# Optimization experiments

Measured on AMD Instinct MI355X. Metric: run time of the kernel, lower is better.

The kernel has to match this reference:

```python
import jax, jax.numpy as jnp
import numpy as np

B, T, D, HEADS = 2, 2048, 1024, 16


def setup_inputs() -> dict:
    key = jax.random.key(0)
    k1, k2, k3 = jax.random.split(key, 3)
    X = jax.random.normal(k1, (B, T, D), dtype=jnp.float32)
    W_KQV = jax.random.normal(k2, (D, 3 * D), dtype=jnp.float32) * 0.02
    W_out = jax.random.normal(k3, (D, D), dtype=jnp.float32) * 0.02
    # causal additive mask: -1e9 above the diagonal, 0 elsewhere
    mask = jnp.triu(jnp.full((T, T), -1e9, dtype=jnp.float32), k=1)
    return {"X": X, "W_KQV": W_KQV, "W_out": W_out, "mask": mask, "heads": HEADS}


def reference(X, W_KQV, W_out, mask, heads):
    b, t, d = X.shape
    hd = d // heads
    res = jnp.einsum('btd,de->bte', X, W_KQV)  # [B,T,3d]
    # needle module stacks split columns in K, Q, V order
    K, Q, V = jnp.split(res, 3, axis=-1)

    def to_heads(A):  # [B,T,d] -> [B,H,T,hd]
        return A.reshape(b, t, heads, hd).transpose(0, 2, 1, 3)

    K, Q, V = to_heads(K), to_heads(Q), to_heads(V)
    # NOTE: original computes K @ Q^T (not Q @ K^T) -- reproduced faithfully
    scores = jnp.einsum('bhkd,bhqd->bhkq', K, Q) / (hd ** 0.5) + mask  # [B,H,T,T]
    attn = jax.nn.softmax(scores, axis=-1)
    ctx = jnp.einsum('bhtq,bhqd->bhtd', attn, V)  # [B,H,T,hd]
    ctx = ctx.transpose(0, 2, 1, 3).reshape(b, t, d)
    out = jnp.einsum('btd,de->bte', ctx, W_out)  # [B,T,d]
    return out, attn
```

## Files before the change

### kernel.cpp

```cpp
#include <hip/hip_runtime.h>
#include <cstddef>

constexpr int B_ = 2, T_ = 2048, D_ = 1024, H_ = 16;

typedef __attribute__((ext_vector_type(8))) short short8;
typedef __attribute__((ext_vector_type(4))) float floatx4;

__device__ inline unsigned short f2bf(float f) {
    union { float f; unsigned int u; } v; v.f = f;
    unsigned int r = v.u + 0x7fffu + ((v.u >> 16) & 1u);
    return (unsigned short)(r >> 16);
}

#define GLD_LDS16(gptr, ldsptr)                                                        \
    __builtin_amdgcn_global_load_lds(                                                  \
        (const __attribute__((address_space(1))) void*)(gptr),                         \
        (__attribute__((address_space(3))) void*)(ldsptr), 16, 0, 0)

__global__ __launch_bounds__(256) void cast_bf16(const float* __restrict__ in,
                                                 unsigned short* __restrict__ out) {
    int idx = (blockIdx.x * 256 + threadIdx.x) * 8;
    float4 a = *(const float4*)(in + idx);
    float4 b = *(const float4*)(in + idx + 4);
    unsigned short tmp[8] = {f2bf(a.x), f2bf(a.y), f2bf(a.z), f2bf(a.w),
                             f2bf(b.x), f2bf(b.y), f2bf(b.z), f2bf(b.w)};
    *(uint4*)(out + idx) = *(const uint4*)tmp;
}

__global__ __launch_bounds__(256) void transpose_cast(const float* __restrict__ W,
                                                      unsigned short* __restrict__ Wt,
                                                      int K, int N) {
    const int k0 = blockIdx.y * 64, n0 = blockIdx.x * 64;
    __shared__ float t[64][65];
    const int tid = threadIdx.x;
    const int row = tid >> 4, c4 = (tid & 15) * 4;
#pragma unroll
    for (int r = 0; r < 4; r++) {
        float4 v = *(const float4*)&W[(size_t)(k0 + row + r * 16) * N + n0 + c4];
        t[row + r * 16][c4 + 0] = v.x; t[row + r * 16][c4 + 1] = v.y;
        t[row + r * 16][c4 + 2] = v.z; t[row + r * 16][c4 + 3] = v.w;
    }
    __syncthreads();
    const int n = tid >> 2, ks = (tid & 3) * 16;
    unsigned short o[16];
#pragma unroll
    for (int i = 0; i < 16; i++) o[i] = f2bf(t[ks + i][n]);
    unsigned short* dst = Wt + (size_t)(n0 + n) * K + k0 + ks;
    *(uint4*)dst = ((const uint4*)o)[0];
    *(uint4*)(dst + 8) = ((const uint4*)o)[1];
}

template <typename CT>
__global__ __launch_bounds__(256, 2) void gemm_bt(const unsigned short* __restrict__ A,
                                                  const unsigned short* __restrict__ Bt,
                                                  CT* __restrict__ C, int M, int N, int K) {
    __shared__ unsigned short As[128 * 64];
    __shared__ unsigned short Bs[128 * 64];
    const int tid = threadIdx.x;
    const int lane = tid & 63, wave = tid >> 6;
    const int quad = lane >> 4, l16 = lane & 15;
    const int wr = wave >> 1, wc = wave & 1;
    const size_t bm = (size_t)blockIdx.y * 128, bn = (size_t)blockIdx.x * 128;
    const unsigned short* Ap = A + bm * K;
    const unsigned short* Bp = Bt + bn * K;
    const int srow = tid >> 3, sc = tid & 7;
    floatx4 acc[4][4] = {};
    for (int k0 = 0; k0 < K; k0 += 64) {
#pragma unroll
        for (int it = 0; it < 4; it++) {
            int rr = srow + it * 32;
            int soff = k0 + ((sc ^ (rr & 7)) << 3);
            GLD_LDS16(Ap + (size_t)rr * K + soff, &As[(tid + it * 256) * 8]);
            GLD_LDS16(Bp + (size_t)rr * K + soff, &Bs[(tid + it * 256) * 8]);
        }
        __syncthreads();
#pragma unroll
        for (int ks = 0; ks < 2; ks++) {
            short8 af[4], bf[4];
#pragma unroll
            for (int i = 0; i < 4; i++) {
                int row = wr * 64 + i * 16 + l16, cf = ks * 4 + quad;
                af[i] = *(const short8*)&As[row * 64 + ((cf ^ (row & 7)) << 3)];
            }
#pragma unroll
            for (int j = 0; j < 4; j++) {
                int row = wc * 64 + j * 16 + l16, cf = ks * 4 + quad;
                bf[j] = *(const short8*)&Bs[row * 64 + ((cf ^ (row & 7)) << 3)];
            }
#pragma unroll
            for (int i = 0; i < 4; i++)
#pragma unroll
                for (int j = 0; j < 4; j++)
                    acc[i][j] = __builtin_amdgcn_mfma_f32_16x16x32_bf16(af[i], bf[j], acc[i][j], 0, 0, 0);
        }
        __syncthreads();
    }
#pragma unroll
    for (int i = 0; i < 4; i++) {
        size_t row0 = bm + wr * 64 + i * 16 + quad * 4;
#pragma unroll
        for (int j = 0; j < 4; j++) {
            size_t col = bn + wc * 64 + j * 16 + l16;
#pragma unroll
            for (int r = 0; r < 4; r++) {
                if constexpr (sizeof(CT) == 2)
                    C[(row0 + r) * N + col] = (CT)f2bf(acc[i][j][r]);
                else
                    C[(row0 + r) * N + col] = acc[i][j][r];
            }
        }
    }
}

__global__ __launch_bounds__(256) void transpose_v(const unsigned short* __restrict__ resb,
                                                   unsigned short* __restrict__ Vt) {
    const int bh = blockIdx.y, b = bh >> 4, h = bh & 15;
    const int q0 = blockIdx.x * 64;
    __shared__ unsigned short t[64][66];
    const int tid = threadIdx.x;
    const unsigned short* Vg = resb + (size_t)b * T_ * (3 * D_) + 2 * D_ + h * 64;
    const int q = tid >> 3, c8 = (tid & 7) * 8;
#pragma unroll
    for (int r = 0; r < 2; r++) {
        int qq = q + r * 32;
        short8 v = *(const short8*)(Vg + (size_t)(q0 + qq) * (3 * D_) + c8);
#pragma unroll
        for (int i = 0; i < 8; i++) t[qq][c8 + i] = (unsigned short)v[i];
    }
    __syncthreads();
    const int c = tid >> 2, qs = (tid & 3) * 16;
    unsigned short o[16];
#pragma unroll
    for (int i = 0; i < 16; i++) o[i] = t[qs + i][c];
    unsigned short* dst = Vt + ((size_t)bh * 64 + c) * T_ + q0 + qs;
    *(uint4*)dst = ((const uint4*)o)[0];
    *(uint4*)(dst + 8) = ((const uint4*)o)[1];
}

__global__ __launch_bounds__(256, 2) void attn_fused(const unsigned short* __restrict__ resb,
                                                     const unsigned short* __restrict__ Vt,
                                                     float* __restrict__ attn,
                                                     unsigned short* __restrict__ ctxb) {
    const int bh = blockIdx.y, b = bh >> 4, h = bh & 15;
    const int xx = (int)blockIdx.x;
    const int kt = (blockIdx.y & 16) ? xx : (15 - xx);
    const int k0 = kt * 128;
    float* S = attn + (size_t)bh * T_ * T_;

    __shared__ char smem[68608];
    unsigned short* Qs = (unsigned short*)smem;
    unsigned short* Ps = (unsigned short*)(smem + 16384);
    unsigned short* Vs = (unsigned short*)(smem + 50176);
    float* lpart = (float*)(smem + 67072);
    float* linv = lpart + 256;

    const int tid = threadIdx.x;
    const int lane = tid & 63, wave = tid >> 6;
    const int quad = lane >> 4, l16 = lane & 15;
    const int wr = wave >> 1, wc = wave & 1;

    const unsigned short* Kg = resb + (size_t)b * T_ * (3 * D_) + h * 64;
    const unsigned short* Qg = Kg + D_;
    const unsigned short* Vg = Vt + (size_t)bh * 64 * T_;

    {
        const int qz0 = (kt + 1) * 128, ZW = T_ - qz0;
        const float4 z = make_float4(0.f, 0.f, 0.f, 0.f);
        for (int row = wave; row < 128; row += 4)
            for (int c = lane * 4; c < ZW; c += 256)
                *(float4*)&S[(size_t)(k0 + row) * T_ + qz0 + c] = z;
    }

    const int srow = tid >> 3, sc = tid & 7;
#pragma unroll
    for (int it = 0; it < 4; it++) {
        int rr = srow + it * 32;
        GLD_LDS16(Kg + (size_t)(k0 + rr) * (3 * D_) + ((sc ^ (rr & 7)) << 3),
                  &Vs[(tid + it * 256) * 8]);
    }
#pragma unroll
    for (int it = 0; it < 4; it++) {
        int rr = srow + it * 32;
        GLD_LDS16(Qg + (size_t)rr * (3 * D_) + ((sc ^ (rr & 7)) << 3),
                  &Qs[(tid + it * 256) * 8]);
    }
    asm volatile("s_waitcnt vmcnt(4)" ::: "memory");
    __builtin_amdgcn_sched_barrier(0);
    __syncthreads();
    short8 af_k[4][2];
#pragma unroll
    for (int i = 0; i < 4; i++)
#pragma unroll
        for (int ks = 0; ks < 2; ks++) {
            int row = wr * 64 + i * 16 + l16, cf = ks * 4 + quad;
            af_k[i][ks] = *(const short8*)&Vs[row * 64 + ((cf ^ (row & 7)) << 3)];
        }

    float l_run[4][4];
#pragma unroll
    for (int i = 0; i < 4; i++)
#pragma unroll
        for (int r = 0; r < 4; r++) l_run[i][r] = 0.f;

    unsigned short* bufA[2] = {Qs, Ps};
    for (int qt = 0; qt <= kt; qt++) {
        if (qt < kt) {
            unsigned short* nb = bufA[(qt + 1) & 1];
            const int q0n = (qt + 1) * 128;
#pragma unroll
            for (int it = 0; it < 4; it++) {
                int rr = srow + it * 32;
                GLD_LDS16(Qg + (size_t)(q0n + rr) * (3 * D_) + ((sc ^ (rr & 7)) << 3),
                          &nb[(tid + it * 256) * 8]);
            }
            asm volatile("s_waitcnt vmcnt(4)" ::: "memory");
        } else {
            asm volatile("s_waitcnt vmcnt(0)" ::: "memory");
        }
        __builtin_amdgcn_sched_barrier(0);
        __syncthreads();
        const unsigned short* cb = bufA[qt & 1];
        short8 bf[4][2];
#pragma unroll
        for (int j = 0; j < 4; j++)
#pragma unroll
            for (int ks = 0; ks < 2; ks++) {
                int row = wc * 64 + j * 16 + l16, cf = ks * 4 + quad;
                bf[j][ks] = *(const short8*)&cb[row * 64 + ((cf ^ (row & 7)) << 3)];
            }
        __syncthreads();
        floatx4 acc[4][4] = {};
        __builtin_amdgcn_s_setprio(1);
#pragma unroll
        for (int ks = 0; ks < 2; ks++)
#pragma unroll
            for (int i = 0; i < 4; i++)
#pragma unroll
                for (int j = 0; j < 4; j++)
                    acc[i][j] = __builtin_amdgcn_mfma_f32_16x16x32_bf16(af_k[i][ks], bf[j][ks], acc[i][j], 0, 0, 0);
        __builtin_amdgcn_s_setprio(0);
        const bool dm = (qt == kt);
#pragma unroll
        for (int i = 0; i < 4; i++)
#pragma unroll
            for (int r = 0; r < 4; r++) {
                const int krow = wr * 64 + i * 16 + quad * 4 + r;
                float e[4];
#pragma unroll
                for (int j = 0; j < 4; j++) {
                    float ex = __expf(acc[i][j][r] * 0.125f);
                    if (dm) {
                        int ql = wc * 64 + j * 16 + l16;
                        if (ql > krow) ex = 0.f;
                    }
                    e[j] = ex;
                }
                l_run[i][r] += (e[0] + e[1]) + (e[2] + e[3]);
            }
    }
#pragma unroll
    for (int i = 0; i < 4; i++)
#pragma unroll
        for (int r = 0; r < 4; r++) {
            float lv = l_run[i][r];
#pragma unroll
            for (int msk = 1; msk < 16; msk <<= 1) lv += __shfl_xor(lv, msk, 64);
            if (l16 == 0) lpart[wc * 128 + wr * 64 + i * 16 + quad * 4 + r] = lv;
        }
    __syncthreads();
    if (tid < 128) linv[tid] = 1.0f / (lpart[tid] + lpart[128 + tid]);
    __syncthreads();

    float li_reg[4][4];
#pragma unroll
    for (int i = 0; i < 4; i++)
#pragma unroll
        for (int r = 0; r < 4; r++)
            li_reg[i][r] = linv[wr * 64 + i * 16 + quad * 4 + r];

    floatx4 cacc[4][2] = {};
#pragma unroll
    for (int it = 0; it < 4; it++) {
        int rr = srow + it * 32;
        GLD_LDS16(Qg + (size_t)rr * (3 * D_) + ((sc ^ (rr & 7)) << 3),
                  &Qs[(tid + it * 256) * 8]);
    }
    short8 vreg[4];
#pragma unroll
    for (int it = 0; it < 4; it++) {
        int ci = tid + it * 256, row = ci >> 4, ch = ci & 15;
        vreg[it] = *(const short8*)&Vg[(size_t)row * T_ + ch * 8];
    }
    for (int qt = 0; qt <= kt; qt++) {
        const int q0 = qt * 128;
        asm volatile("s_waitcnt vmcnt(0)" ::: "memory");
        __builtin_amdgcn_sched_barrier(0);
#pragma unroll
        for (int it = 0; it < 4; it++) {
            int ci = tid + it * 256, row = ci >> 4, ch = ci & 15;
            *(short8*)&Vs[row * 132 + ch * 8] = vreg[it];
        }
        __syncthreads();
        short8 bf[4][2];
#pragma unroll
        for (int j = 0; j < 4; j++)
#pragma unroll
            for (int ks = 0; ks < 2; ks++) {
                int row = wc * 64 + j * 16 + l16, cf = ks * 4 + quad;
                bf[j][ks] = *(const short8*)&Qs[row * 64 + ((cf ^ (row & 7)) << 3)];
            }
        __syncthreads();
        if (qt < kt) {
            const int q0n = q0 + 128;
#pragma unroll
            for (int it = 0; it < 4; it++) {
                int rr = srow + it * 32;
                GLD_LDS16(Qg + (size_t)(q0n + rr) * (3 * D_) + ((sc ^ (rr & 7)) << 3),
                          &Qs[(tid + it * 256) * 8]);
            }
#pragma unroll
            for (int it = 0; it < 4; it++) {
                int ci = tid + it * 256, row = ci >> 4, ch = ci & 15;
                vreg[it] = *(const short8*)&Vg[(size_t)row * T_ + q0n + ch * 8];
            }
        }
        __builtin_amdgcn_sched_barrier(0);
        floatx4 acc[4][4] = {};
        __builtin_amdgcn_s_setprio(1);
#pragma unroll
        for (int ks = 0; ks < 2; ks++)
#pragma unroll
            for (int i = 0; i < 4; i++)
#pragma unroll
                for (int j = 0; j < 4; j++)
                    acc[i][j] = __builtin_amdgcn_mfma_f32_16x16x32_bf16(af_k[i][ks], bf[j][ks], acc[i][j], 0, 0, 0);
        __builtin_amdgcn_s_setprio(0);
        const bool dm = (qt == kt);
#pragma unroll
        for (int i = 0; i < 4; i++)
#pragma unroll
            for (int r = 0; r < 4; r++) {
                const int krow = wr * 64 + i * 16 + quad * 4 + r;
                const float li = li_reg[i][r];
#pragma unroll
                for (int j = 0; j < 4; j++) {
                    int ql = wc * 64 + j * 16 + l16;
                    float p = __expf(acc[i][j][r] * 0.125f) * li;
                    if (dm && ql > krow) p = 0.f;
                    S[(size_t)(k0 + krow) * T_ + q0 + ql] = p;
                    Ps[krow * 132 + ql] = f2bf(p);
                }
            }
        __syncthreads();
        __builtin_amdgcn_s_setprio(1);
#pragma unroll
        for (int ks2 = 0; ks2 < 4; ks2++) {
            short8 ap[4], bv[2];
#pragma unroll
            for (int i = 0; i < 4; i++)
                ap[i] = *(const short8*)&Ps[(wr * 64 + i * 16 + l16) * 132 + ks2 * 32 + quad * 8];
#pragma unroll
            for (int j2 = 0; j2 < 2; j2++)
                bv[j2] = *(const short8*)&Vs[(wc * 32 + j2 * 16 + l16) * 132 + ks2 * 32 + quad * 8];
#pragma unroll
            for (int i = 0; i < 4; i++)
#pragma unroll
                for (int j2 = 0; j2 < 2; j2++)
                    cacc[i][j2] = __builtin_amdgcn_mfma_f32_16x16x32_bf16(ap[i], bv[j2], cacc[i][j2], 0, 0, 0);
        }
        __builtin_amdgcn_s_setprio(0);
        __syncthreads();
    }
#pragma unroll
    for (int i = 0; i < 4; i++) {
        size_t t0 = (size_t)k0 + wr * 64 + i * 16 + quad * 4;
#pragma unroll
        for (int j2 = 0; j2 < 2; j2++) {
            int c = wc * 32 + j2 * 16 + l16;
#pragma unroll
            for (int r = 0; r < 4; r++)
                ctxb[((size_t)b * T_ + t0 + r) * D_ + h * 64 + c] = f2bf(cacc[i][j2][r]);
        }
    }
}

extern "C" void kernel_launch(void* const* d_in, const int* in_sizes, int n_in,
                              void* d_out, int out_size, void* d_ws, size_t ws_size,
                              hipStream_t stream) {
    const float* X = (const float*)d_in[0];
    const float* W_KQV = (const float*)d_in[1];
    const float* W_out = (const float*)d_in[2];
    float* out = (float*)d_out;
    float* attn = (float*)d_out + (size_t)B_ * T_ * D_;

    char* ws = (char*)d_ws;
    unsigned short* Xb = (unsigned short*)ws;
    unsigned short* Wt = (unsigned short*)(ws + (8u << 20));
    unsigned short* Wot = (unsigned short*)(ws + (14u << 20));
    unsigned short* resb = (unsigned short*)(ws + (16u << 20));
    unsigned short* Vt = (unsigned short*)(ws + (40u << 20));
    unsigned short* ctxb = (unsigned short*)(ws + (48u << 20));

    cast_bf16<<<(B_ * T_ * D_) / (8 * 256), 256, 0, stream>>>(X, Xb);
    transpose_cast<<<dim3((3 * D_) / 64, D_ / 64), 256, 0, stream>>>(W_KQV, Wt, D_, 3 * D_);
    transpose_cast<<<dim3(D_ / 64, D_ / 64), 256, 0, stream>>>(W_out, Wot, D_, D_);

    gemm_bt<unsigned short><<<dim3((3 * D_) / 128, (B_ * T_) / 128), 256, 0, stream>>>(
        Xb, Wt, resb, B_ * T_, 3 * D_, D_);

    transpose_v<<<dim3(T_ / 64, B_ * H_), 256, 0, stream>>>(resb, Vt);

    attn_fused<<<dim3(16, B_ * H_), 256, 0, stream>>>(resb, Vt, attn, ctxb);

    gemm_bt<float><<<dim3(D_ / 128, (B_ * T_) / 128), 256, 0, stream>>>(
        ctxb, Wot, out, B_ * T_, D_, D_);
}
```

Baseline: 785.3 us.

## Fuse V transpose into attention kernel and use exp2 with folded scale

Removes the separate transpose_v kernel and its workspace buffer. The attention kernel now reads V rows directly from the QKV projection output and transposes them while scattering into LDS. The V prefetch is moved ahead of the row-sum reduction, and the wait before the first loop iteration is relaxed to vmcnt(63) on later iterations so loads overlap more. exp is replaced by exp2f with the log2(e)/8 scale folded in. The cost is scalar strided LDS stores for V, which may cause bank conflicts.

Measured after the change: 791.2 us. About the same (+0.7%).

```diff
diff --git a/kernel.cpp b/kernel.cpp
--- a/kernel.cpp
+++ b/kernel.cpp
@@ -16,6 +16,8 @@
     __builtin_amdgcn_global_load_lds(                                                  \
         (const __attribute__((address_space(1))) void*)(gptr),                         \
         (__attribute__((address_space(3))) void*)(ldsptr), 16, 0, 0)
+
+#define EXP_SCALE 0.18033688011118324f
 
 __global__ __launch_bounds__(256) void cast_bf16(const float* __restrict__ in,
                                                  unsigned short* __restrict__ out) {
@@ -112,33 +114,7 @@
     }
 }
 
-__global__ __launch_bounds__(256) void transpose_v(const unsigned short* __restrict__ resb,
-                                                   unsigned short* __restrict__ Vt) {
-    const int bh = blockIdx.y, b = bh >> 4, h = bh & 15;
-    const int q0 = blockIdx.x * 64;
-    __shared__ unsigned short t[64][66];
-    const int tid = threadIdx.x;
-    const unsigned short* Vg = resb + (size_t)b * T_ * (3 * D_) + 2 * D_ + h * 64;
-    const int q = tid >> 3, c8 = (tid & 7) * 8;
-#pragma unroll
-    for (int r = 0; r < 2; r++) {
-        int qq = q + r * 32;
-        short8 v = *(const short8*)(Vg + (size_t)(q0 + qq) * (3 * D_) + c8);
-#pragma unroll
-        for (int i = 0; i < 8; i++) t[qq][c8 + i] = (unsigned short)v[i];
-    }
-    __syncthreads();
-    const int c = tid >> 2, qs = (tid & 3) * 16;
-    unsigned short o[16];
-#pragma unroll
-    for (int i = 0; i < 16; i++) o[i] = t[qs + i][c];
-    unsigned short* dst = Vt + ((size_t)bh * 64 + c) * T_ + q0 + qs;
-    *(uint4*)dst = ((const uint4*)o)[0];
-    *(uint4*)(dst + 8) = ((const uint4*)o)[1];
-}
-
 __global__ __launch_bounds__(256, 2) void attn_fused(const unsigned short* __restrict__ resb,
-                                                     const unsigned short* __restrict__ Vt,
                                                      float* __restrict__ attn,
                                                      unsigned short* __restrict__ ctxb) {
     const int bh = blockIdx.y, b = bh >> 4, h = bh & 15;
@@ -161,7 +137,7 @@
 
     const unsigned short* Kg = resb + (size_t)b * T_ * (3 * D_) + h * 64;
     const unsigned short* Qg = Kg + D_;
-    const unsigned short* Vg = Vt + (size_t)bh * 64 * T_;
+    const unsigned short* Vg = Kg + 2 * D_;
 
     {
         const int qz0 = (kt + 1) * 128, ZW = T_ - qz0;
@@ -248,7 +224,7 @@
                 float e[4];
 #pragma unroll
                 for (int j = 0; j < 4; j++) {
-                    float ex = __expf(acc[i][j][r] * 0.125f);
+                    float ex = exp2f(acc[i][j][r] * EXP_SCALE);
                     if (dm) {
                         int ql = wc * 64 + j * 16 + l16;
                         if (ql > krow) ex = 0.f;
@@ -258,27 +234,7 @@
                 l_run[i][r] += (e[0] + e[1]) + (e[2] + e[3]);
             }
     }
-#pragma unroll
-    for (int i = 0; i < 4; i++)
-#pragma unroll
-        for (int r = 0; r < 4; r++) {
-            float lv = l_run[i][r];
-#pragma unroll
-            for (int msk = 1; msk < 16; msk <<= 1) lv += __shfl_xor(lv, msk, 64);
-            if (l16 == 0) lpart[wc * 128 + wr * 64 + i * 16 + quad * 4 + r] = lv;
-        }
-    __syncthreads();
-    if (tid < 128) linv[tid] = 1.0f / (lpart[tid] + lpart[128 + tid]);
-    __syncthreads();
-
-    float li_reg[4][4];
-#pragma unroll
-    for (int i = 0; i < 4; i++)
-#pragma unroll
-        for (int r = 0; r < 4; r++)
-            li_reg[i][r] = linv[wr * 64 + i * 16 + quad * 4 + r];
-
-    floatx4 cacc[4][2] = {};
+
 #pragma unroll
     for (int it = 0; it < 4; it++) {
         int rr = srow + it * 32;
@@ -288,17 +244,42 @@
     short8 vreg[4];
 #pragma unroll
     for (int it = 0; it < 4; it++) {
-        int ci = tid + it * 256, row = ci >> 4, ch = ci & 15;
-        vreg[it] = *(const short8*)&Vg[(size_t)row * T_ + ch * 8];
-    }
+        int qq = (tid >> 3) + it * 32, c8 = (tid & 7) * 8;
+        vreg[it] = *(const short8*)&Vg[(size_t)qq * (3 * D_) + c8];
+    }
+
+#pragma unroll
+    for (int i = 0; i < 4; i++)
+#pragma unroll
+        for (int r = 0; r < 4; r++) {
+            float lv = l_run[i][r];
+#pragma unroll
+            for (int msk = 1; msk < 16; msk <<= 1) lv += __shfl_xor(lv, msk, 64);
+            if (l16 == 0) lpart[wc * 128 + wr * 64 + i * 16 + quad * 4 + r] = lv;
+        }
+    __syncthreads();
+    if (tid < 128) linv[tid] = 1.0f / (lpart[tid] + lpart[128 + tid]);
+    __syncthreads();
+
+    float li_reg[4][4];
+#pragma unroll
+    for (int i = 0; i < 4; i++)
+#pragma unroll
+        for (int r = 0; r < 4; r++)
+            li_reg[i][r] = linv[wr * 64 + i * 16 + quad * 4 + r];
+
+    floatx4 cacc[4][2] = {};
     for (int qt = 0; qt <= kt; qt++) {
         const int q0 = qt * 128;
-        asm volatile("s_waitcnt vmcnt(0)" ::: "memory");
+        if (qt == 0) asm volatile("s_waitcnt vmcnt(0)" ::: "memory");
+        else         asm volatile("s_waitcnt vmcnt(63)" ::: "memory");
         __builtin_amdgcn_sched_barrier(0);
 #pragma unroll
         for (int it = 0; it < 4; it++) {
-            int ci = tid + it * 256, row = ci >> 4, ch = ci & 15;
-            *(short8*)&Vs[row * 132 + ch * 8] = vreg[it];
+            int qq = (tid >> 3) + it * 32, c8 = (tid & 7) * 8;
+#pragma unroll
+            for (int i = 0; i < 8; i++)
+                Vs[(c8 + i) * 132 + qq] = (unsigned short)vreg[it][i];
         }
         __syncthreads();
         short8 bf[4][2];
@@ -320,8 +301,8 @@
             }
 #pragma unroll
             for (int it = 0; it < 4; it++) {
-                int ci = tid + it * 256, row = ci >> 4, ch = ci & 15;
-                vreg[it] = *(const short8*)&Vg[(size_t)row * T_ + q0n + ch * 8];
+                int qq = (tid >> 3) + it * 32, c8 = (tid & 7) * 8;
+                vreg[it] = *(const short8*)&Vg[(size_t)(q0n + qq) * (3 * D_) + c8];
             }
         }
         __builtin_amdgcn_sched_barrier(0);
@@ -345,7 +326,7 @@
 #pragma unroll
                 for (int j = 0; j < 4; j++) {
                     int ql = wc * 64 + j * 16 + l16;
-                    float p = __expf(acc[i][j][r] * 0.125f) * li;
+                    float p = exp2f(acc[i][j][r] * EXP_SCALE) * li;
                     if (dm && ql > krow) p = 0.f;
                     S[(size_t)(k0 + krow) * T_ + q0 + ql] = p;
                     Ps[krow * 132 + ql] = f2bf(p);
@@ -398,7 +379,6 @@
     unsigned short* Wt = (unsigned short*)(ws + (8u << 20));
     unsigned short* Wot = (unsigned short*)(ws + (14u << 20));
     unsigned short* resb = (unsigned short*)(ws + (16u << 20));
-    unsigned short* Vt = (unsigned short*)(ws + (40u << 20));
     unsigned short* ctxb = (unsigned short*)(ws + (48u << 20));
 
     cast_bf16<<<(B_ * T_ * D_) / (8 * 256), 256, 0, stream>>>(X, Xb);
@@ -408,9 +388,7 @@
     gemm_bt<unsigned short><<<dim3((3 * D_) / 128, (B_ * T_) / 128), 256, 0, stream>>>(
         Xb, Wt, resb, B_ * T_, 3 * D_, D_);
 
-    transpose_v<<<dim3(T_ / 64, B_ * H_), 256, 0, stream>>>(resb, Vt);
-
-    attn_fused<<<dim3(16, B_ * H_), 256, 0, stream>>>(resb, Vt, attn, ctxb);
+    attn_fused<<<dim3(16, B_ * H_), 256, 0, stream>>>(resb, attn, ctxb);
 
     gemm_bt<float><<<dim3(D_ / 128, (B_ * T_) / 128), 256, 0, stream>>>(
         ctxb, Wot, out, B_ * T_, D_, D_);
```
